# Kernel tuning notes

Hardware: AMD Instinct MI355X
Metric: run time of the kernel (lower is better)

## Reference

```python
import jax, jax.numpy as jnp
import numpy as np
import math

N_QUBITS = 14
STATE = 2 ** N_QUBITS  # 16384
BATCH = 512

# binary_matrix(n)[i, j] == bit (n-1-i) of j  (row-major reshape of [2]*n cube)
_BITS = ((jnp.arange(STATE)[None, :] >> (N_QUBITS - 1 - jnp.arange(N_QUBITS))[:, None]) & 1).astype(jnp.float32)  # [n, 2**n]


def setup_inputs() -> dict:
    key = jax.random.key(0)
    k1, k2, k3 = jax.random.split(key, 3)
    phi_real = jax.random.normal(k1, (BATCH, STATE), dtype=jnp.float32)
    phi_imag = jax.random.normal(k2, (BATCH, STATE), dtype=jnp.float32)
    thetas = jax.random.normal(k3, (BATCH, N_QUBITS), dtype=jnp.float32)
    return {"phi_real": phi_real, "phi_imag": phi_imag, "thetas": thetas}


def _fwht(x):
    """Fast Walsh-Hadamard transform over last dim (butterfly, same math as had_big).
    Order of the per-qubit butterflies is irrelevant for the full transform."""
    B, N = x.shape
    h = 1
    while h < N:
        xr = x.reshape(B, N // (2 * h), 2, h)
        a, b = xr[:, :, 0, :], xr[:, :, 1, :]
        x = jnp.stack([a + b, a - b], axis=2).reshape(B, N)
        h *= 2
    n = int(math.log2(N))
    return x * jnp.asarray(2.0 ** (-n / 2), dtype=jnp.float32)


def reference(phi_real, phi_imag, thetas):
    phi = phi_real + 1j * phi_imag  # complex64 state [B, 2**n]
    # RZ eigenvalues: exp(-i * (thetas @ binary_mask) / 2), first (only) chunk
    phase = thetas @ _BITS  # [B, 2**n]
    ev = jnp.exp(-0.5j * phase.astype(jnp.complex64))
    phi = _fwht(phi)
    phi = phi * ev
    phi = _fwht(phi)
    return phi
```

## Files before the change

### kernel.cpp

```cpp
#include <hip/hip_runtime.h>

#define NQ 14
#define STATE 16384
#define BATCH 512
#define THREADS 512
#define PER 32
#define SCALE 6.103515625e-05f

__device__ __forceinline__ int swz(int row, int col) {
    return (row << 7) + (col ^ ((row & 7) << 2));
}

template <int MAXM>
__device__ __forceinline__ void fwht_regs(float (&x)[PER]) {
#pragma unroll
    for (int m = 1; m <= MAXM; m <<= 1) {
#pragma unroll
        for (int r = 0; r < PER; ++r) {
            if (!(r & m)) {
                float a = x[r], b = x[r | m];
                x[r] = a + b;
                x[r | m] = a - b;
            }
        }
    }
}


__device__ __forceinline__ void wr_L0(float* lds, const float (&x)[PER], int t) {
#pragma unroll
    for (int i = 0; i < 8; ++i) {
        float4 v = make_float4(x[4 * i], x[4 * i + 1], x[4 * i + 2], x[4 * i + 3]);
        *(float4*)&lds[swz(i * 16 + (t >> 5), (t & 31) * 4)] = v;
    }
}
__device__ __forceinline__ void rd_L0(const float* lds, float (&x)[PER], int t) {
#pragma unroll
    for (int i = 0; i < 8; ++i) {
        float4 v = *(const float4*)&lds[swz(i * 16 + (t >> 5), (t & 31) * 4)];
        x[4 * i] = v.x; x[4 * i + 1] = v.y; x[4 * i + 2] = v.z; x[4 * i + 3] = v.w;
    }
}
__device__ __forceinline__ void wr_L1(float* lds, const float (&x)[PER], int t) {
    const int row = t >> 2, base = t & 3;
#pragma unroll
    for (int r = 0; r < PER; ++r) lds[swz(row, r * 4 + base)] = x[r];
}
__device__ __forceinline__ void rd_L1(const float* lds, float (&x)[PER], int t) {
    const int row = t >> 2, base = t & 3;
#pragma unroll
    for (int r = 0; r < PER; ++r) x[r] = lds[swz(row, r * 4 + base)];
}
__device__ __forceinline__ void wr_L2(float* lds, const float (&x)[PER], int t) {
    const int rowb = (t >> 6) * 16;
    const int colb = ((t >> 2) & 15) * 4 + (t & 3);
#pragma unroll
    for (int r = 0; r < PER; ++r)
        lds[swz(rowb + (r & 15), (r >> 4) * 64 + colb)] = x[r];
}
__device__ __forceinline__ void rd_L2(const float* lds, float (&x)[PER], int t) {
    const int rowb = (t >> 6) * 16;
    const int colb = ((t >> 2) & 15) * 4 + (t & 3);
#pragma unroll
    for (int r = 0; r < PER; ++r)
        x[r] = lds[swz(rowb + (r & 15), (r >> 4) * 64 + colb)];
}

#define XCHG(WR, RD)                                        \
    do {                                                    \
        WR(lds, re, t); __syncthreads();                    \
        RD(lds, re, t); __syncthreads();                    \
        WR(lds, im, t); __syncthreads();                    \
        RD(lds, im, t); __syncthreads();                    \
    } while (0)

__global__ void __launch_bounds__(THREADS, 4)
rx_kernel(const float* __restrict__ phr, const float* __restrict__ phim,
          const float* __restrict__ th, float* __restrict__ out,
          long long out_limit) {
    __shared__ float lds[STATE];
    const int b = blockIdx.x;
    const int t = threadIdx.x;
    float re[PER], im[PER];

    const float* pr = phr + (size_t)b * STATE;
    const float* pi = phim + (size_t)b * STATE;
#pragma unroll
    for (int i = 0; i < 8; ++i) {
        float4 a = *(const float4*)(pr + i * 2048 + t * 4);
        float4 c = *(const float4*)(pi + i * 2048 + t * 4);
        re[4 * i] = a.x; re[4 * i + 1] = a.y; re[4 * i + 2] = a.z; re[4 * i + 3] = a.w;
        im[4 * i] = c.x; im[4 * i + 1] = c.y; im[4 * i + 2] = c.z; im[4 * i + 3] = c.w;
    }
    float w[NQ];
#pragma unroll
    for (int k = 0; k < NQ; ++k) w[k] = th[b * NQ + 13 - k];

    fwht_regs<16>(re); fwht_regs<16>(im);
    XCHG(wr_L0, rd_L1);
    fwht_regs<16>(re); fwht_regs<16>(im);
    XCHG(wr_L1, rd_L2);
    fwht_regs<8>(re);  fwht_regs<8>(im);

    float tp = 0.f;
    if (t & 1)   tp += w[0];
    if (t & 2)   tp += w[1];
    if (t & 4)   tp += w[2];
    if (t & 8)   tp += w[3];
    if (t & 16)  tp += w[4];
    if (t & 32)  tp += w[5];
    if (t & 64)  tp += w[11];
    if (t & 128) tp += w[12];
    if (t & 256) tp += w[13];
#pragma unroll
    for (int r = 0; r < PER; ++r) {
        float ph = tp;
        if (r & 1)  ph += w[7];
        if (r & 2)  ph += w[8];
        if (r & 4)  ph += w[9];
        if (r & 8)  ph += w[10];
        if (r & 16) ph += w[6];
        const float ang = -0.5f * ph;
        float sn = __sinf(ang) * SCALE;
        float cs = __cosf(ang) * SCALE;
        float nr = re[r] * cs - im[r] * sn;
        float ni = re[r] * sn + im[r] * cs;
        re[r] = nr; im[r] = ni;
    }

    fwht_regs<8>(re);  fwht_regs<8>(im);
    XCHG(wr_L2, rd_L1);
    fwht_regs<16>(re); fwht_regs<16>(im);
    XCHG(wr_L1, rd_L0);
    fwht_regs<16>(re); fwht_regs<16>(im);

    if (out_limit == (long long)BATCH * STATE) {
        float* o = out + (size_t)b * STATE;
        const long long base = (long long)b * STATE;
#pragma unroll
        for (int i = 0; i < 8; ++i) {
            const int s0 = i * 2048 + t * 4;
            if (base + s0 + 3 < out_limit)
                *(float4*)(o + s0) = make_float4(re[4 * i], re[4 * i + 1],
                                                 re[4 * i + 2], re[4 * i + 3]);
        }
    } else {
        float* ore = out + (size_t)b * STATE;
        float* oim = out + (size_t)BATCH * STATE + (size_t)b * STATE;
        const long long bre = (long long)b * STATE;
        const long long bim = (long long)BATCH * STATE + bre;
#pragma unroll
        for (int i = 0; i < 8; ++i) {
            const int s0 = i * 2048 + t * 4;
            if (bre + s0 + 3 < out_limit)
                *(float4*)(ore + s0) = make_float4(re[4 * i], re[4 * i + 1],
                                                   re[4 * i + 2], re[4 * i + 3]);
            if (bim + s0 + 3 < out_limit)
                *(float4*)(oim + s0) = make_float4(im[4 * i], im[4 * i + 1],
                                                   im[4 * i + 2], im[4 * i + 3]);
        }
    }
}

extern "C" void kernel_launch(void* const* d_in, const int* in_sizes, int n_in,
                              void* d_out, int out_size, void* d_ws, size_t ws_size,
                              hipStream_t stream) {
    const float* phr  = (const float*)d_in[0];
    const float* phim = (const float*)d_in[1];
    const float* th   = (const float*)d_in[2];
    float* out = (float*)d_out;
    rx_kernel<<<BATCH, THREADS, 0, stream>>>(phr, phim, th, out,
                                             (long long)out_size);
}
```

Before: 118.1 us.

## Pack re/im into float2 vectors, pad LDS rows, drop intra-wave barriers

Stores each complex amplitude as a two-float vector so the Walsh-Hadamard butterflies can use packed f32 add/sub on both components at once. The XOR swizzle is replaced by a row stride padded to 132 words, held in dynamic shared memory. The two middle exchanges (L1 to L2 and back) lose all __syncthreads, because each 64-thread wavefront reads only the rows it wrote itself. This cuts barrier stalls and ALU instruction count. In exchange the kernel uses slightly more LDS and relies on wavefront-local ordering of LDS operations for correctness.

After: 113.5 us. 3.9% less time.

```diff
diff --git a/kernel.cpp b/kernel.cpp
--- a/kernel.cpp
+++ b/kernel.cpp
@@ -5,20 +5,22 @@
 #define BATCH 512
 #define THREADS 512
 #define PER 32
+#define STRIDE 132
+#define LDS_WORDS (128 * STRIDE)
 #define SCALE 6.103515625e-05f
 
-__device__ __forceinline__ int swz(int row, int col) {
-    return (row << 7) + (col ^ ((row & 7) << 2));
-}
+typedef float v2f __attribute__((ext_vector_type(2)));
+
+__device__ __forceinline__ int adr(int row, int col) { return row * STRIDE + col; }
 
 template <int MAXM>
-__device__ __forceinline__ void fwht_regs(float (&x)[PER]) {
+__device__ __forceinline__ void fwht_pk(v2f (&x)[PER]) {
 #pragma unroll
     for (int m = 1; m <= MAXM; m <<= 1) {
 #pragma unroll
         for (int r = 0; r < PER; ++r) {
             if (!(r & m)) {
-                float a = x[r], b = x[r | m];
+                v2f a = x[r], b = x[r | m];
                 x[r] = a + b;
                 x[r | m] = a - b;
             }
@@ -27,61 +29,55 @@
 }
 
 
-__device__ __forceinline__ void wr_L0(float* lds, const float (&x)[PER], int t) {
+template <int C>
+__device__ __forceinline__ void wrL0(float* lds, const v2f (&x)[PER], int t) {
 #pragma unroll
     for (int i = 0; i < 8; ++i) {
-        float4 v = make_float4(x[4 * i], x[4 * i + 1], x[4 * i + 2], x[4 * i + 3]);
-        *(float4*)&lds[swz(i * 16 + (t >> 5), (t & 31) * 4)] = v;
-    }
-}
-__device__ __forceinline__ void rd_L0(const float* lds, float (&x)[PER], int t) {
+        float4 v = make_float4(x[4 * i][C], x[4 * i + 1][C], x[4 * i + 2][C], x[4 * i + 3][C]);
+        *(float4*)&lds[adr(i * 16 + (t >> 5), (t & 31) * 4)] = v;
+    }
+}
+template <int C>
+__device__ __forceinline__ void rdL0(const float* lds, v2f (&x)[PER], int t) {
 #pragma unroll
     for (int i = 0; i < 8; ++i) {
-        float4 v = *(const float4*)&lds[swz(i * 16 + (t >> 5), (t & 31) * 4)];
-        x[4 * i] = v.x; x[4 * i + 1] = v.y; x[4 * i + 2] = v.z; x[4 * i + 3] = v.w;
-    }
-}
-__device__ __forceinline__ void wr_L1(float* lds, const float (&x)[PER], int t) {
-    const int row = t >> 2, base = t & 3;
-#pragma unroll
-    for (int r = 0; r < PER; ++r) lds[swz(row, r * 4 + base)] = x[r];
-}
-__device__ __forceinline__ void rd_L1(const float* lds, float (&x)[PER], int t) {
-    const int row = t >> 2, base = t & 3;
-#pragma unroll
-    for (int r = 0; r < PER; ++r) x[r] = lds[swz(row, r * 4 + base)];
-}
-__device__ __forceinline__ void wr_L2(float* lds, const float (&x)[PER], int t) {
-    const int rowb = (t >> 6) * 16;
-    const int colb = ((t >> 2) & 15) * 4 + (t & 3);
-#pragma unroll
-    for (int r = 0; r < PER; ++r)
-        lds[swz(rowb + (r & 15), (r >> 4) * 64 + colb)] = x[r];
-}
-__device__ __forceinline__ void rd_L2(const float* lds, float (&x)[PER], int t) {
-    const int rowb = (t >> 6) * 16;
-    const int colb = ((t >> 2) & 15) * 4 + (t & 3);
-#pragma unroll
-    for (int r = 0; r < PER; ++r)
-        x[r] = lds[swz(rowb + (r & 15), (r >> 4) * 64 + colb)];
-}
-
-#define XCHG(WR, RD)                                        \
-    do {                                                    \
-        WR(lds, re, t); __syncthreads();                    \
-        RD(lds, re, t); __syncthreads();                    \
-        WR(lds, im, t); __syncthreads();                    \
-        RD(lds, im, t); __syncthreads();                    \
-    } while (0)
+        float4 v = *(const float4*)&lds[adr(i * 16 + (t >> 5), (t & 31) * 4)];
+        x[4 * i][C] = v.x; x[4 * i + 1][C] = v.y; x[4 * i + 2][C] = v.z; x[4 * i + 3][C] = v.w;
+    }
+}
+template <int C>
+__device__ __forceinline__ void wrL1(float* lds, const v2f (&x)[PER], int t) {
+    const int base = adr(t >> 2, t & 3);
+#pragma unroll
+    for (int r = 0; r < PER; ++r) lds[base + r * 4] = x[r][C];
+}
+template <int C>
+__device__ __forceinline__ void rdL1(const float* lds, v2f (&x)[PER], int t) {
+    const int base = adr(t >> 2, t & 3);
+#pragma unroll
+    for (int r = 0; r < PER; ++r) x[r][C] = lds[base + r * 4];
+}
+template <int C>
+__device__ __forceinline__ void wrL2(float* lds, const v2f (&x)[PER], int t) {
+    const int base = adr((t >> 6) * 16, ((t >> 2) & 15) * 4 + (t & 3));
+#pragma unroll
+    for (int r = 0; r < PER; ++r) lds[base + (r & 15) * STRIDE + (r >> 4) * 64] = x[r][C];
+}
+template <int C>
+__device__ __forceinline__ void rdL2(const float* lds, v2f (&x)[PER], int t) {
+    const int base = adr((t >> 6) * 16, ((t >> 2) & 15) * 4 + (t & 3));
+#pragma unroll
+    for (int r = 0; r < PER; ++r) x[r][C] = lds[base + (r & 15) * STRIDE + (r >> 4) * 64];
+}
 
 __global__ void __launch_bounds__(THREADS, 4)
 rx_kernel(const float* __restrict__ phr, const float* __restrict__ phim,
           const float* __restrict__ th, float* __restrict__ out,
           long long out_limit) {
-    __shared__ float lds[STATE];
+    extern __shared__ float lds[];
     const int b = blockIdx.x;
     const int t = threadIdx.x;
-    float re[PER], im[PER];
+    v2f x[PER];
 
     const float* pr = phr + (size_t)b * STATE;
     const float* pi = phim + (size_t)b * STATE;
@@ -89,18 +85,33 @@
     for (int i = 0; i < 8; ++i) {
         float4 a = *(const float4*)(pr + i * 2048 + t * 4);
         float4 c = *(const float4*)(pi + i * 2048 + t * 4);
-        re[4 * i] = a.x; re[4 * i + 1] = a.y; re[4 * i + 2] = a.z; re[4 * i + 3] = a.w;
-        im[4 * i] = c.x; im[4 * i + 1] = c.y; im[4 * i + 2] = c.z; im[4 * i + 3] = c.w;
+        x[4 * i]     = v2f{a.x, c.x};
+        x[4 * i + 1] = v2f{a.y, c.y};
+        x[4 * i + 2] = v2f{a.z, c.z};
+        x[4 * i + 3] = v2f{a.w, c.w};
     }
     float w[NQ];
 #pragma unroll
     for (int k = 0; k < NQ; ++k) w[k] = th[b * NQ + 13 - k];
 
-    fwht_regs<16>(re); fwht_regs<16>(im);
-    XCHG(wr_L0, rd_L1);
-    fwht_regs<16>(re); fwht_regs<16>(im);
-    XCHG(wr_L1, rd_L2);
-    fwht_regs<8>(re);  fwht_regs<8>(im);
+    fwht_pk<16>(x);
+
+    wrL0<0>(lds, x, t);
+    __syncthreads();
+    rdL1<0>(lds, x, t);
+    __syncthreads();
+    wrL0<1>(lds, x, t);
+    __syncthreads();
+    rdL1<1>(lds, x, t);
+
+    fwht_pk<16>(x);
+
+    wrL1<0>(lds, x, t);
+    rdL2<0>(lds, x, t);
+    wrL1<1>(lds, x, t);
+    rdL2<1>(lds, x, t);
+
+    fwht_pk<8>(x);
 
     float tp = 0.f;
     if (t & 1)   tp += w[0];
@@ -123,16 +134,29 @@
         const float ang = -0.5f * ph;
         float sn = __sinf(ang) * SCALE;
         float cs = __cosf(ang) * SCALE;
-        float nr = re[r] * cs - im[r] * sn;
-        float ni = re[r] * sn + im[r] * cs;
-        re[r] = nr; im[r] = ni;
-    }
-
-    fwht_regs<8>(re);  fwht_regs<8>(im);
-    XCHG(wr_L2, rd_L1);
-    fwht_regs<16>(re); fwht_regs<16>(im);
-    XCHG(wr_L1, rd_L0);
-    fwht_regs<16>(re); fwht_regs<16>(im);
+        float nr = x[r][0] * cs - x[r][1] * sn;
+        float ni = x[r][0] * sn + x[r][1] * cs;
+        x[r] = v2f{nr, ni};
+    }
+
+    fwht_pk<8>(x);
+
+    wrL2<0>(lds, x, t);
+    rdL1<0>(lds, x, t);
+    wrL2<1>(lds, x, t);
+    rdL1<1>(lds, x, t);
+
+    fwht_pk<16>(x);
+
+    wrL1<0>(lds, x, t);
+    __syncthreads();
+    rdL0<0>(lds, x, t);
+    __syncthreads();
+    wrL1<1>(lds, x, t);
+    __syncthreads();
+    rdL0<1>(lds, x, t);
+
+    fwht_pk<16>(x);
 
     if (out_limit == (long long)BATCH * STATE) {
         float* o = out + (size_t)b * STATE;
@@ -141,8 +165,8 @@
         for (int i = 0; i < 8; ++i) {
             const int s0 = i * 2048 + t * 4;
             if (base + s0 + 3 < out_limit)
-                *(float4*)(o + s0) = make_float4(re[4 * i], re[4 * i + 1],
-                                                 re[4 * i + 2], re[4 * i + 3]);
+                *(float4*)(o + s0) = make_float4(x[4 * i][0], x[4 * i + 1][0],
+                                                 x[4 * i + 2][0], x[4 * i + 3][0]);
         }
     } else {
         float* ore = out + (size_t)b * STATE;
@@ -153,11 +177,11 @@
         for (int i = 0; i < 8; ++i) {
             const int s0 = i * 2048 + t * 4;
             if (bre + s0 + 3 < out_limit)
-                *(float4*)(ore + s0) = make_float4(re[4 * i], re[4 * i + 1],
-                                                   re[4 * i + 2], re[4 * i + 3]);
+                *(float4*)(ore + s0) = make_float4(x[4 * i][0], x[4 * i + 1][0],
+                                                   x[4 * i + 2][0], x[4 * i + 3][0]);
             if (bim + s0 + 3 < out_limit)
-                *(float4*)(oim + s0) = make_float4(im[4 * i], im[4 * i + 1],
-                                                   im[4 * i + 2], im[4 * i + 3]);
+                *(float4*)(oim + s0) = make_float4(x[4 * i][1], x[4 * i + 1][1],
+                                                   x[4 * i + 2][1], x[4 * i + 3][1]);
         }
     }
 }
@@ -169,6 +193,9 @@
     const float* phim = (const float*)d_in[1];
     const float* th   = (const float*)d_in[2];
     float* out = (float*)d_out;
-    rx_kernel<<<BATCH, THREADS, 0, stream>>>(phr, phim, th, out,
-                                             (long long)out_size);
-}
+    (void)hipFuncSetAttribute((const void*)rx_kernel,
+                              hipFuncAttributeMaxDynamicSharedMemorySize,
+                              LDS_WORDS * (int)sizeof(float));
+    rx_kernel<<<BATCH, THREADS, LDS_WORDS * sizeof(float), stream>>>(
+        phr, phim, th, out, (long long)out_size);
+}
```
